# Kernel tuning notes

Measured on AMD Instinct MI355X. Metric: run time of the kernel, lower is better.

Reference implementation:

```python
import jax, jax.numpy as jnp
import numpy as np

N_NODES = 100000
N_EDGES = 1600000
D = 128
RESIDUAL_WEIGHT = 0.001


def setup_inputs() -> dict:
    key = jax.random.key(0)
    k = jax.random.split(key, 7)
    x = jax.random.normal(k[0], (N_NODES, D), dtype=jnp.float32)
    edge_index = jax.random.randint(k[1], (2, N_EDGES), 0, N_NODES, dtype=jnp.int32)
    s = 1.0 / np.sqrt(D)
    Wl = jax.random.normal(k[2], (D, D), dtype=jnp.float32) * s
    bl = jax.random.normal(k[3], (D,), dtype=jnp.float32) * s
    Wr = jax.random.normal(k[4], (D, D), dtype=jnp.float32) * s
    Wres = jax.random.normal(k[5], (D, D), dtype=jnp.float32) * s
    bres = jax.random.normal(k[6], (D,), dtype=jnp.float32) * s
    return {"x": x, "edge_index": edge_index, "Wl": Wl, "bl": bl,
            "Wr": Wr, "Wres": Wres, "bres": bres}


def reference(x, edge_index, Wl, bl, Wr, Wres, bres):
    # PyG SAGEConv(aggr='sum'): messages x_j flow src -> dst
    src, dst = edge_index[0], edge_index[1]
    agg = jax.ops.segment_sum(x[src], dst, num_segments=x.shape[0])  # [N, D]
    # lin_l(agg) (with bias) + lin_r(x) (root weight, no bias)
    h_sage = agg @ Wl.T + bl + x @ Wr.T
    # residual Linear
    h_res = x @ Wres.T + bres
    rw = jnp.float32(RESIDUAL_WEIGHT)
    # dropout p=0 (eval) -> identity
    return rw * h_sage + (1.0 - rw) * h_res
```

## Files before the change

kernel.cpp:

```cpp
#include <hip/hip_runtime.h>
#include <hip/hip_bf16.h>
#include <stdint.h>

#define DD 128
#define RW 0.001f
#define CHUNK 4096
#define CAP 4096
#define YSCALE 256.0f
#define YINV (1.0f/256.0f)

typedef __attribute__((ext_vector_type(4))) float f32x4;
typedef __attribute__((ext_vector_type(2))) float f32x2;
typedef __attribute__((ext_vector_type(8))) short bf16x8;

static __device__ __forceinline__ uint32_t pack2(float lo, float hi){
  return __builtin_amdgcn_perm(__float_as_uint(hi), __float_as_uint(lo), 0x07060302u);
}

static __device__ __forceinline__ ushort rne_bf16(float f){
  uint32_t u = __float_as_uint(f);
  return (ushort)((u + 0x7fffu + ((u >> 16) & 1u)) >> 16);
}

__global__ void prep_weights(const float* __restrict__ Wl, const float* __restrict__ bl,
                             const float* __restrict__ Wr, const float* __restrict__ Wres,
                             const float* __restrict__ bres,
                             ushort* __restrict__ Wlb, ushort* __restrict__ Wcb,
                             float* __restrict__ bc){
  int i = blockIdx.x * 256 + threadIdx.x;
  float wl = RW * Wl[i];
  float wc = RW * Wr[i] + (1.f - RW) * Wres[i];
  Wlb[i] = rne_bf16(wl);
  Wcb[i] = rne_bf16(wc);
  if (i < DD) bc[i] = RW * bl[i] + (1.f - RW) * bres[i];
}

__global__ __launch_bounds__(512) void bfill(const int* __restrict__ src,
                                             const int* __restrict__ dst,
                                             int* __restrict__ gcnt,
                                             uint32_t* __restrict__ recs, int E, int nb){
  __shared__ uint32_t srec[CHUNK];
  __shared__ uint16_t sb[CHUNK];
  __shared__ int hcnt[800];
  __shared__ int hbase[800];
  __shared__ int lcur[800];
  int t = threadIdx.x;
  int base = blockIdx.x * CHUNK;
  for (int i = t; i < nb; i += 512){ hcnt[i] = 0; lcur[i] = 0; }
  __syncthreads();
  #pragma unroll
  for (int k = 0; k < 8; k++){
    int idx = k * 512 + t;
    int e = base + idx;
    uint16_t b = 0xFFFFu;
    if (e < E){
      int d = dst[e];
      b = (uint16_t)(d >> 7);
      srec[idx] = ((uint32_t)(d & 127) << 17) | (uint32_t)src[e];
      atomicAdd(&hcnt[b], 1);
    }
    sb[idx] = b;
  }
  __syncthreads();
  for (int i = t; i < nb; i += 512)
    hbase[i] = hcnt[i] ? atomicAdd(&gcnt[i], hcnt[i]) : 0;
  __syncthreads();
  #pragma unroll
  for (int k = 0; k < 8; k++){
    int idx = k * 512 + t;
    uint16_t b = sb[idx];
    if (b != 0xFFFFu){
      int p = hbase[b] + atomicAdd(&lcur[b], 1);
      if (p < CAP) recs[(size_t)b * CAP + p] = srec[idx];
    }
  }
}

__global__ __launch_bounds__(512) void bsort(uint32_t* __restrict__ recs,
                                             const int* __restrict__ gcnt,
                                             int* __restrict__ nstart,
                                             int* __restrict__ ncnt, int M){
  __shared__ uint32_t srec[CAP];
  __shared__ uint32_t ssorted[CAP];
  __shared__ int h[128], pstart[128], lc[128];
  int t = threadIdx.x;
  int b = blockIdx.x;
  int s = b * CAP;
  int cnt = gcnt[b];
  if (cnt > CAP) cnt = CAP;

  if (t < 128){ h[t] = 0; lc[t] = 0; }
  __syncthreads();
  for (int i = t; i < cnt; i += 512){
    uint32_t r = recs[s + i];
    srec[i] = r;
    atomicAdd(&h[(r >> 17) & 127u], 1);
  }
  __syncthreads();
  int val = (t < 128) ? h[t] : 0;
  #pragma unroll
  for (int off = 1; off < 128; off <<= 1){
    if (t < 128) pstart[t] = val;
    __syncthreads();
    if (t < 128 && t >= off) val += pstart[t - off];
    __syncthreads();
  }
  if (t < 128){
    pstart[t] = val - h[t];
    int node = b * 128 + t;
    if (node < M){
      nstart[node] = s + pstart[t];
      ncnt[node]  = h[t];
    }
  }
  __syncthreads();
  for (int i = t; i < cnt; i += 512){
    uint32_t r = srec[i];
    int n7 = (int)((r >> 17) & 127u);
    int pos = pstart[n7] + atomicAdd(&lc[n7], 1);
    ssorted[pos] = r & 0x1FFFFu;
  }
  __syncthreads();
  for (int i = t; i < cnt; i += 512)
    recs[s + i] = ssorted[i];
}

__global__ __launch_bounds__(512, 4) void gemm_fused(
    const float* __restrict__ x, const ushort* __restrict__ Wlb,
    const ushort* __restrict__ Wcb, const float* __restrict__ bc,
    uint8_t* __restrict__ y, float* __restrict__ out, int M)
{
  __shared__ char sX[32768];
  int tid = threadIdx.x;

  #pragma unroll
  for (int p = 0; p < 4; p++){
    int g   = p * 512 + tid;
    int row = g >> 4;
    int cb  = (tid & 15) * 16;
    int grow = blockIdx.x * 128 + row;
    if (grow >= M) grow = M - 1;
    const float* ap = x + (size_t)grow * DD + (tid & 15) * 8;
    f32x4 f0 = *(const f32x4*)ap;
    f32x4 f1 = *(const f32x4*)(ap + 4);
    uint4 wv;
    wv.x = pack2(f0[0], f0[1]);
    wv.y = pack2(f0[2], f0[3]);
    wv.z = pack2(f1[0], f1[1]);
    wv.w = pack2(f1[2], f1[3]);
    int sw = (row << 8) | (cb ^ ((row & 7) << 4));
    *(uint4*)&sX[sw] = wv;
  }
  __syncthreads();

  int lane = tid & 63, w = tid >> 6;
  int wr = w >> 2, wc = w & 3;
  int l15 = lane & 15, lhi = lane >> 4;
  int rowbase = blockIdx.x * 128 + wr * 64;
  int mtx = wc >> 1;
  int colbase = (wc & 1) * 64;
  const ushort* Wb = mtx ? Wcb : Wlb;

  f32x4 acc[4][4];
  #pragma unroll
  for (int a = 0; a < 4; a++)
    #pragma unroll
    for (int b = 0; b < 4; b++) acc[a][b] = (f32x4){0.f,0.f,0.f,0.f};

  #pragma unroll
  for (int ks = 0; ks < 4; ks++){
    bf16x8 afr[4];
    #pragma unroll
    for (int rt = 0; rt < 4; rt++){
      int row = wr * 64 + rt * 16 + l15;
      int byte = (row << 8) | ((ks * 64 + lhi * 16) ^ ((row & 7) << 4));
      afr[rt] = *(const bf16x8*)&sX[byte];
    }
    #pragma unroll
    for (int ct = 0; ct < 4; ct++){
      int colm = colbase + ct * 16 + l15;
      bf16x8 bfr = *(const bf16x8*)(Wb + (size_t)colm * DD + ks * 32 + lhi * 8);
      #pragma unroll
      for (int rt = 0; rt < 4; rt++)
        acc[rt][ct] = __builtin_amdgcn_mfma_f32_16x16x32_bf16(bfr, afr[rt], acc[rt][ct], 0, 0, 0);
    }
  }

  if (mtx == 1){
    #pragma unroll
    for (int ct = 0; ct < 4; ct++){
      int col = colbase + ct * 16 + lhi * 4;
      f32x4 b4 = *(const f32x4*)&bc[col];
      #pragma unroll
      for (int rt = 0; rt < 4; rt++){
        int row = rowbase + rt * 16 + l15;
        if (row < M){
          f32x4 o = acc[rt][ct] + b4;
          *(f32x4*)(out + (size_t)row * DD + col) = o;
        }
      }
    }
  } else {
    #pragma unroll
    for (int ct = 0; ct < 4; ct++){
      int col = colbase + ct * 16 + lhi * 4;
      #pragma unroll
      for (int rt = 0; rt < 4; rt++){
        int row = rowbase + rt * 16 + l15;
        if (row < M){
          int pk = __builtin_amdgcn_cvt_pk_fp8_f32(acc[rt][ct][0] * YSCALE,
                                                   acc[rt][ct][1] * YSCALE, 0, false);
          pk = __builtin_amdgcn_cvt_pk_fp8_f32(acc[rt][ct][2] * YSCALE,
                                               acc[rt][ct][3] * YSCALE, pk, true);
          *(uint32_t*)(y + (size_t)row * DD + col) = (uint32_t)pk;
        }
      }
    }
  }
}

__global__ __launch_bounds__(256) void agg_add(
    const uint8_t* __restrict__ y, const uint32_t* __restrict__ csr,
    const int* __restrict__ nstart, const int* __restrict__ ncnt,
    float* __restrict__ out, int N)
{
  int wid = (int)((blockIdx.x * 256 + threadIdx.x) >> 6);
  if (wid >= N) return;
  int lane = threadIdx.x & 63;
  int start = nstart[wid], cnt = ncnt[wid];
  float a0 = 0.f, a1 = 0.f, b0 = 0.f, b1 = 0.f;
  float c0 = 0.f, c1 = 0.f, d0 = 0.f, d1 = 0.f;
  int i = 0;
  for (; i + 8 <= cnt; i += 8){
    int s0 = (int)csr[start + i];
    int s1 = (int)csr[start + i + 1];
    int s2 = (int)csr[start + i + 2];
    int s3 = (int)csr[start + i + 3];
    int s4 = (int)csr[start + i + 4];
    int s5 = (int)csr[start + i + 5];
    int s6 = (int)csr[start + i + 6];
    int s7 = (int)csr[start + i + 7];
    int v0 = *(const ushort*)(y + (size_t)s0 * DD + lane * 2);
    int v1 = *(const ushort*)(y + (size_t)s1 * DD + lane * 2);
    int v2 = *(const ushort*)(y + (size_t)s2 * DD + lane * 2);
    int v3 = *(const ushort*)(y + (size_t)s3 * DD + lane * 2);
    int v4 = *(const ushort*)(y + (size_t)s4 * DD + lane * 2);
    int v5 = *(const ushort*)(y + (size_t)s5 * DD + lane * 2);
    int v6 = *(const ushort*)(y + (size_t)s6 * DD + lane * 2);
    int v7 = *(const ushort*)(y + (size_t)s7 * DD + lane * 2);
    f32x2 f0 = __builtin_amdgcn_cvt_pk_f32_fp8(v0, false);
    f32x2 f1 = __builtin_amdgcn_cvt_pk_f32_fp8(v1, false);
    f32x2 f2 = __builtin_amdgcn_cvt_pk_f32_fp8(v2, false);
    f32x2 f3 = __builtin_amdgcn_cvt_pk_f32_fp8(v3, false);
    f32x2 f4 = __builtin_amdgcn_cvt_pk_f32_fp8(v4, false);
    f32x2 f5 = __builtin_amdgcn_cvt_pk_f32_fp8(v5, false);
    f32x2 f6 = __builtin_amdgcn_cvt_pk_f32_fp8(v6, false);
    f32x2 f7 = __builtin_amdgcn_cvt_pk_f32_fp8(v7, false);
    a0 += f0[0] + f4[0]; a1 += f0[1] + f4[1];
    b0 += f1[0] + f5[0]; b1 += f1[1] + f5[1];
    c0 += f2[0] + f6[0]; c1 += f2[1] + f6[1];
    d0 += f3[0] + f7[0]; d1 += f3[1] + f7[1];
  }
  for (; i + 2 <= cnt; i += 2){
    int s0 = (int)csr[start + i];
    int s1 = (int)csr[start + i + 1];
    int v0 = *(const ushort*)(y + (size_t)s0 * DD + lane * 2);
    int v1 = *(const ushort*)(y + (size_t)s1 * DD + lane * 2);
    f32x2 f0 = __builtin_amdgcn_cvt_pk_f32_fp8(v0, false);
    f32x2 f1 = __builtin_amdgcn_cvt_pk_f32_fp8(v1, false);
    a0 += f0[0]; a1 += f0[1];
    b0 += f1[0]; b1 += f1[1];
  }
  if (i < cnt){
    int s0 = (int)csr[start + i];
    int v0 = *(const ushort*)(y + (size_t)s0 * DD + lane * 2);
    f32x2 f0 = __builtin_amdgcn_cvt_pk_f32_fp8(v0, false);
    a0 += f0[0]; a1 += f0[1];
  }
  a0 = (a0 + b0 + c0 + d0) * YINV;
  a1 = (a1 + b1 + c1 + d1) * YINV;
  float2* p = (float2*)(out + (size_t)wid * DD + lane * 2);
  float2 t = *p;
  t.x += a0; t.y += a1;
  *p = t;
}

extern "C" void kernel_launch(void* const* d_in, const int* in_sizes, int n_in,
                              void* d_out, int out_size, void* d_ws, size_t ws_size,
                              hipStream_t stream) {
  const float* x    = (const float*)d_in[0];
  const int*   ei   = (const int*)d_in[1];
  const float* Wl   = (const float*)d_in[2];
  const float* bl   = (const float*)d_in[3];
  const float* Wr   = (const float*)d_in[4];
  const float* Wres = (const float*)d_in[5];
  const float* bres = (const float*)d_in[6];
  float* out = (float*)d_out;

  int M = in_sizes[0] / DD;
  int E = in_sizes[1] / 2;
  const int* esrc = ei;
  const int* edst = ei + E;
  int nb = (M + 127) >> 7;

  char* wsp = (char*)d_ws;
  size_t off = 0;
  uint8_t*  y    = (uint8_t*) (wsp + off); off += (size_t)M * DD;      off = (off + 255) & ~255ull;
  uint32_t* recs = (uint32_t*)(wsp + off); off += (size_t)800 * CAP * 4;
  ushort*   Wlb  = (ushort*)  (wsp + off); off += DD * DD * 2;
  ushort*   Wcb  = (ushort*)  (wsp + off); off += DD * DD * 2;
  float*    bc   = (float*)   (wsp + off); off += 512;
  int*      gcnt = (int*)     (wsp + off); off += sizeof(int) * 1024;
  int*      nstart=(int*)     (wsp + off); off += sizeof(int) * (size_t)M; off = (off + 255) & ~255ull;
  int*      ncnt = (int*)     (wsp + off); off += sizeof(int) * (size_t)M;

  hipMemsetAsync(gcnt, 0, sizeof(int) * 1024, stream);
  prep_weights<<<(DD * DD) / 256, 256, 0, stream>>>(Wl, bl, Wr, Wres, bres, Wlb, Wcb, bc);
  int nchunk = (E + CHUNK - 1) / CHUNK;
  bfill<<<nchunk, 512, 0, stream>>>(esrc, edst, gcnt, recs, E, nb);
  bsort<<<nb, 512, 0, stream>>>(recs, gcnt, nstart, ncnt, M);
  gemm_fused<<<(M + 127) / 128, 512, 0, stream>>>(x, Wlb, Wcb, bc, y, out, M);
  agg_add<<<((size_t)M * 64 + 255) / 256, 256, 0, stream>>>(y, recs, nstart, ncnt, out, M);
}
```

Before: 135.5 us.

## Aggregate quantized x before GEMM and fuse both linear maps into one kernel

Reorders the computation from transform-then-aggregate to aggregate-then-transform. x is first quantized to fp8, neighbour sums are gathered into an fp8 ybar buffer, and a single GEMM over the concatenated [x | ybar] input with a fused 128x256 weight writes the output. This drops the read-modify-write of out in the old aggregation pass, and the aggregation now splits each node's edges across two waves. In exchange it adds a quantization kernel and an extra M*128 byte intermediate, and fp8 rounding of raw x and of the summed aggregate may reduce accuracy.

```diff
diff --git a/kernel.cpp b/kernel.cpp
--- a/kernel.cpp
+++ b/kernel.cpp
@@ -6,8 +6,7 @@
 #define RW 0.001f
 #define CHUNK 4096
 #define CAP 4096
-#define YSCALE 256.0f
-#define YINV (1.0f/256.0f)
+#define YS 8.0f
 
 typedef __attribute__((ext_vector_type(4))) float f32x4;
 typedef __attribute__((ext_vector_type(2))) float f32x2;
@@ -25,14 +24,28 @@
 __global__ void prep_weights(const float* __restrict__ Wl, const float* __restrict__ bl,
                              const float* __restrict__ Wr, const float* __restrict__ Wres,
                              const float* __restrict__ bres,
-                             ushort* __restrict__ Wlb, ushort* __restrict__ Wcb,
-                             float* __restrict__ bc){
+                             ushort* __restrict__ Wfb, float* __restrict__ bc){
   int i = blockIdx.x * 256 + threadIdx.x;
-  float wl = RW * Wl[i];
-  float wc = RW * Wr[i] + (1.f - RW) * Wres[i];
-  Wlb[i] = rne_bf16(wl);
-  Wcb[i] = rne_bf16(wc);
+  int c = i >> 8, k = i & 255;
+  float v;
+  if (k < DD) v = RW * Wr[c * DD + k] + (1.f - RW) * Wres[c * DD + k];
+  else        v = (RW / YS) * Wl[c * DD + (k - DD)];
+  Wfb[i] = rne_bf16(v);
   if (i < DD) bc[i] = RW * bl[i] + (1.f - RW) * bres[i];
+}
+
+__global__ __launch_bounds__(256) void quantx(const float* __restrict__ x,
+                                              uint8_t* __restrict__ xb, int n8){
+  int i = blockIdx.x * 256 + threadIdx.x;
+  if (i >= n8) return;
+  const f32x4* p = (const f32x4*)(x + (size_t)i * 8);
+  f32x4 f0 = p[0], f1 = p[1];
+  int pk0 = __builtin_amdgcn_cvt_pk_fp8_f32(f0[0], f0[1], 0, false);
+  pk0     = __builtin_amdgcn_cvt_pk_fp8_f32(f0[2], f0[3], pk0, true);
+  int pk1 = __builtin_amdgcn_cvt_pk_fp8_f32(f1[0], f1[1], 0, false);
+  pk1     = __builtin_amdgcn_cvt_pk_fp8_f32(f1[2], f1[3], pk1, true);
+  uint2 w; w.x = (uint32_t)pk0; w.y = (uint32_t)pk1;
+  *(uint2*)(xb + (size_t)i * 8) = w;
 }
 
 __global__ __launch_bounds__(512) void bfill(const int* __restrict__ src,
@@ -125,22 +138,108 @@
     recs[s + i] = ssorted[i];
 }
 
-__global__ __launch_bounds__(512, 4) void gemm_fused(
-    const float* __restrict__ x, const ushort* __restrict__ Wlb,
-    const ushort* __restrict__ Wcb, const float* __restrict__ bc,
-    uint8_t* __restrict__ y, float* __restrict__ out, int M)
+__global__ __launch_bounds__(512) void agg(const uint8_t* __restrict__ xb,
+                                           const uint32_t* __restrict__ csr,
+                                           const int* __restrict__ nstart,
+                                           const int* __restrict__ ncnt,
+                                           uint8_t* __restrict__ ybar, int N)
+{
+  __shared__ float2 part[8][64];
+  int t = threadIdx.x;
+  int w = t >> 6, lane = t & 63;
+  int node = blockIdx.x * 4 + (w >> 1);
+  int half = w & 1;
+  float a0 = 0.f, a1 = 0.f, b0 = 0.f, b1 = 0.f;
+  float c0 = 0.f, c1 = 0.f, d0 = 0.f, d1 = 0.f;
+  if (node < N){
+    int start = nstart[node], cnt = ncnt[node];
+    int h = (cnt + 1) >> 1;
+    int i0 = start + half * h;
+    int i1 = start + cnt; if (i0 + h < i1) i1 = i0 + h;
+    int i = i0;
+    for (; i + 8 <= i1; i += 8){
+      int s0 = (int)csr[i];     int s1 = (int)csr[i + 1];
+      int s2 = (int)csr[i + 2]; int s3 = (int)csr[i + 3];
+      int s4 = (int)csr[i + 4]; int s5 = (int)csr[i + 5];
+      int s6 = (int)csr[i + 6]; int s7 = (int)csr[i + 7];
+      int v0 = *(const ushort*)(xb + (size_t)s0 * DD + lane * 2);
+      int v1 = *(const ushort*)(xb + (size_t)s1 * DD + lane * 2);
+      int v2 = *(const ushort*)(xb + (size_t)s2 * DD + lane * 2);
+      int v3 = *(const ushort*)(xb + (size_t)s3 * DD + lane * 2);
+      int v4 = *(const ushort*)(xb + (size_t)s4 * DD + lane * 2);
+      int v5 = *(const ushort*)(xb + (size_t)s5 * DD + lane * 2);
+      int v6 = *(const ushort*)(xb + (size_t)s6 * DD + lane * 2);
+      int v7 = *(const ushort*)(xb + (size_t)s7 * DD + lane * 2);
+      f32x2 f0 = __builtin_amdgcn_cvt_pk_f32_fp8(v0, false);
+      f32x2 f1 = __builtin_amdgcn_cvt_pk_f32_fp8(v1, false);
+      f32x2 f2 = __builtin_amdgcn_cvt_pk_f32_fp8(v2, false);
+      f32x2 f3 = __builtin_amdgcn_cvt_pk_f32_fp8(v3, false);
+      f32x2 f4 = __builtin_amdgcn_cvt_pk_f32_fp8(v4, false);
+      f32x2 f5 = __builtin_amdgcn_cvt_pk_f32_fp8(v5, false);
+      f32x2 f6 = __builtin_amdgcn_cvt_pk_f32_fp8(v6, false);
+      f32x2 f7 = __builtin_amdgcn_cvt_pk_f32_fp8(v7, false);
+      a0 += f0[0] + f4[0]; a1 += f0[1] + f4[1];
+      b0 += f1[0] + f5[0]; b1 += f1[1] + f5[1];
+      c0 += f2[0] + f6[0]; c1 += f2[1] + f6[1];
+      d0 += f3[0] + f7[0]; d1 += f3[1] + f7[1];
+    }
+    for (; i + 2 <= i1; i += 2){
+      int s0 = (int)csr[i];
+      int s1 = (int)csr[i + 1];
+      int v0 = *(const ushort*)(xb + (size_t)s0 * DD + lane * 2);
+      int v1 = *(const ushort*)(xb + (size_t)s1 * DD + lane * 2);
+      f32x2 f0 = __builtin_amdgcn_cvt_pk_f32_fp8(v0, false);
+      f32x2 f1 = __builtin_amdgcn_cvt_pk_f32_fp8(v1, false);
+      a0 += f0[0]; a1 += f0[1];
+      b0 += f1[0]; b1 += f1[1];
+    }
+    if (i < i1){
+      int s0 = (int)csr[i];
+      int v0 = *(const ushort*)(xb + (size_t)s0 * DD + lane * 2);
+      f32x2 f0 = __builtin_amdgcn_cvt_pk_f32_fp8(v0, false);
+      a0 += f0[0]; a1 += f0[1];
+    }
+    a0 += b0 + c0 + d0;
+    a1 += b1 + c1 + d1;
+  }
+  part[w][lane] = (float2){a0, a1};
+  __syncthreads();
+  if (half == 0 && node < N){
+    float2 o = part[w + 1][lane];
+    a0 = (a0 + o.x) * YS;
+    a1 = (a1 + o.y) * YS;
+    int pk = __builtin_amdgcn_cvt_pk_fp8_f32(a0, a1, 0, false);
+    *(ushort*)(ybar + (size_t)node * DD + lane * 2) = (ushort)(pk & 0xFFFF);
+  }
+}
+
+__global__ __launch_bounds__(512, 4) void gemm2(
+    const float* __restrict__ x, const uint8_t* __restrict__ ybar,
+    const ushort* __restrict__ Wfb, const float* __restrict__ bc,
+    float* __restrict__ out, int M)
 {
   __shared__ char sX[32768];
   int tid = threadIdx.x;
+  int lane = tid & 63, w = tid >> 6;
+  int wr = w >> 2, wcol = w & 3;
+  int l15 = lane & 15, lhi = lane >> 4;
+  int rowbase = blockIdx.x * 128 + wr * 64;
+  int colbase = wcol * 32;
+
+  f32x4 acc[4][2];
+  #pragma unroll
+  for (int a = 0; a < 4; a++)
+    #pragma unroll
+    for (int b = 0; b < 2; b++) acc[a][b] = (f32x4){0.f,0.f,0.f,0.f};
 
   #pragma unroll
   for (int p = 0; p < 4; p++){
     int g   = p * 512 + tid;
     int row = g >> 4;
-    int cb  = (tid & 15) * 16;
+    int cx  = tid & 15;
     int grow = blockIdx.x * 128 + row;
     if (grow >= M) grow = M - 1;
-    const float* ap = x + (size_t)grow * DD + (tid & 15) * 8;
+    const float* ap = x + (size_t)grow * DD + cx * 8;
     f32x4 f0 = *(const f32x4*)ap;
     f32x4 f1 = *(const f32x4*)(ap + 4);
     uint4 wv;
@@ -148,24 +247,10 @@
     wv.y = pack2(f0[2], f0[3]);
     wv.z = pack2(f1[0], f1[1]);
     wv.w = pack2(f1[2], f1[3]);
-    int sw = (row << 8) | (cb ^ ((row & 7) << 4));
+    int sw = (row << 8) | ((cx * 16) ^ ((row & 7) << 4));
     *(uint4*)&sX[sw] = wv;
   }
   __syncthreads();
-
-  int lane = tid & 63, w = tid >> 6;
-  int wr = w >> 2, wc = w & 3;
-  int l15 = lane & 15, lhi = lane >> 4;
-  int rowbase = blockIdx.x * 128 + wr * 64;
-  int mtx = wc >> 1;
-  int colbase = (wc & 1) * 64;
-  const ushort* Wb = mtx ? Wcb : Wlb;
-
-  f32x4 acc[4][4];
-  #pragma unroll
-  for (int a = 0; a < 4; a++)
-    #pragma unroll
-    for (int b = 0; b < 4; b++) acc[a][b] = (f32x4){0.f,0.f,0.f,0.f};
 
   #pragma unroll
   for (int ks = 0; ks < 4; ks++){
@@ -177,112 +262,70 @@
       afr[rt] = *(const bf16x8*)&sX[byte];
     }
     #pragma unroll
-    for (int ct = 0; ct < 4; ct++){
+    for (int ct = 0; ct < 2; ct++){
       int colm = colbase + ct * 16 + l15;
-      bf16x8 bfr = *(const bf16x8*)(Wb + (size_t)colm * DD + ks * 32 + lhi * 8);
+      bf16x8 bfr = *(const bf16x8*)(Wfb + (size_t)colm * 256 + ks * 32 + lhi * 8);
       #pragma unroll
       for (int rt = 0; rt < 4; rt++)
         acc[rt][ct] = __builtin_amdgcn_mfma_f32_16x16x32_bf16(bfr, afr[rt], acc[rt][ct], 0, 0, 0);
     }
   }
-
-  if (mtx == 1){
-    #pragma unroll
-    for (int ct = 0; ct < 4; ct++){
-      int col = colbase + ct * 16 + lhi * 4;
-      f32x4 b4 = *(const f32x4*)&bc[col];
+  __syncthreads();
+
+  #pragma unroll
+  for (int p = 0; p < 4; p++){
+    int g   = p * 512 + tid;
+    int row = g >> 4;
+    int cx  = tid & 15;
+    int grow = blockIdx.x * 128 + row;
+    if (grow >= M) grow = M - 1;
+    uint2 rv = *(const uint2*)(ybar + (size_t)grow * DD + cx * 8);
+    f32x2 e0 = __builtin_amdgcn_cvt_pk_f32_fp8((int)rv.x, false);
+    f32x2 e1 = __builtin_amdgcn_cvt_pk_f32_fp8((int)rv.x, true);
+    f32x2 e2 = __builtin_amdgcn_cvt_pk_f32_fp8((int)rv.y, false);
+    f32x2 e3 = __builtin_amdgcn_cvt_pk_f32_fp8((int)rv.y, true);
+    uint4 wv;
+    wv.x = pack2(e0[0], e0[1]);
+    wv.y = pack2(e1[0], e1[1]);
+    wv.z = pack2(e2[0], e2[1]);
+    wv.w = pack2(e3[0], e3[1]);
+    int sw = (row << 8) | ((cx * 16) ^ ((row & 7) << 4));
+    *(uint4*)&sX[sw] = wv;
+  }
+  __syncthreads();
+
+  #pragma unroll
+  for (int ks = 0; ks < 4; ks++){
+    bf16x8 afr[4];
+    #pragma unroll
+    for (int rt = 0; rt < 4; rt++){
+      int row = wr * 64 + rt * 16 + l15;
+      int byte = (row << 8) | ((ks * 64 + lhi * 16) ^ ((row & 7) << 4));
+      afr[rt] = *(const bf16x8*)&sX[byte];
+    }
+    #pragma unroll
+    for (int ct = 0; ct < 2; ct++){
+      int colm = colbase + ct * 16 + l15;
+      bf16x8 bfr = *(const bf16x8*)(Wfb + (size_t)colm * 256 + 128 + ks * 32 + lhi * 8);
       #pragma unroll
-      for (int rt = 0; rt < 4; rt++){
-        int row = rowbase + rt * 16 + l15;
-        if (row < M){
-          f32x4 o = acc[rt][ct] + b4;
-          *(f32x4*)(out + (size_t)row * DD + col) = o;
-        }
+      for (int rt = 0; rt < 4; rt++)
+        acc[rt][ct] = __builtin_amdgcn_mfma_f32_16x16x32_bf16(bfr, afr[rt], acc[rt][ct], 0, 0, 0);
+    }
+  }
+
+  #pragma unroll
+  for (int ct = 0; ct < 2; ct++){
+    int col = colbase + ct * 16 + lhi * 4;
+    f32x4 b4 = *(const f32x4*)&bc[col];
+    #pragma unroll
+    for (int rt = 0; rt < 4; rt++){
+      int row = rowbase + rt * 16 + l15;
+      if (row < M){
+        f32x4 o = acc[rt][ct] + b4;
+        *(f32x4*)(out + (size_t)row * DD + col) = o;
       }
     }
-  } else {
-    #pragma unroll
-    for (int ct = 0; ct < 4; ct++){
-      int col = colbase + ct * 16 + lhi * 4;
-      #pragma unroll
-      for (int rt = 0; rt < 4; rt++){
-        int row = rowbase + rt * 16 + l15;
-        if (row < M){
-          int pk = __builtin_amdgcn_cvt_pk_fp8_f32(acc[rt][ct][0] * YSCALE,
-                                                   acc[rt][ct][1] * YSCALE, 0, false);
-          pk = __builtin_amdgcn_cvt_pk_fp8_f32(acc[rt][ct][2] * YSCALE,
-                                               acc[rt][ct][3] * YSCALE, pk, true);
-          *(uint32_t*)(y + (size_t)row * DD + col) = (uint32_t)pk;
-        }
-      }
-    }
-  }
-}
-
-__global__ __launch_bounds__(256) void agg_add(
-    const uint8_t* __restrict__ y, const uint32_t* __restrict__ csr,
-    const int* __restrict__ nstart, const int* __restrict__ ncnt,
-    float* __restrict__ out, int N)
-{
-  int wid = (int)((blockIdx.x * 256 + threadIdx.x) >> 6);
-  if (wid >= N) return;
-  int lane = threadIdx.x & 63;
-  int start = nstart[wid], cnt = ncnt[wid];
-  float a0 = 0.f, a1 = 0.f, b0 = 0.f, b1 = 0.f;
-  float c0 = 0.f, c1 = 0.f, d0 = 0.f, d1 = 0.f;
-  int i = 0;
-  for (; i + 8 <= cnt; i += 8){
-    int s0 = (int)csr[start + i];
-    int s1 = (int)csr[start + i + 1];
-    int s2 = (int)csr[start + i + 2];
-    int s3 = (int)csr[start + i + 3];
-    int s4 = (int)csr[start + i + 4];
-    int s5 = (int)csr[start + i + 5];
-    int s6 = (int)csr[start + i + 6];
-    int s7 = (int)csr[start + i + 7];
-    int v0 = *(const ushort*)(y + (size_t)s0 * DD + lane * 2);
-    int v1 = *(const ushort*)(y + (size_t)s1 * DD + lane * 2);
-    int v2 = *(const ushort*)(y + (size_t)s2 * DD + lane * 2);
-    int v3 = *(const ushort*)(y + (size_t)s3 * DD + lane * 2);
-    int v4 = *(const ushort*)(y + (size_t)s4 * DD + lane * 2);
-    int v5 = *(const ushort*)(y + (size_t)s5 * DD + lane * 2);
-    int v6 = *(const ushort*)(y + (size_t)s6 * DD + lane * 2);
-    int v7 = *(const ushort*)(y + (size_t)s7 * DD + lane * 2);
-    f32x2 f0 = __builtin_amdgcn_cvt_pk_f32_fp8(v0, false);
-    f32x2 f1 = __builtin_amdgcn_cvt_pk_f32_fp8(v1, false);
-    f32x2 f2 = __builtin_amdgcn_cvt_pk_f32_fp8(v2, false);
-    f32x2 f3 = __builtin_amdgcn_cvt_pk_f32_fp8(v3, false);
-    f32x2 f4 = __builtin_amdgcn_cvt_pk_f32_fp8(v4, false);
-    f32x2 f5 = __builtin_amdgcn_cvt_pk_f32_fp8(v5, false);
-    f32x2 f6 = __builtin_amdgcn_cvt_pk_f32_fp8(v6, false);
-    f32x2 f7 = __builtin_amdgcn_cvt_pk_f32_fp8(v7, false);
-    a0 += f0[0] + f4[0]; a1 += f0[1] + f4[1];
-    b0 += f1[0] + f5[0]; b1 += f1[1] + f5[1];
-    c0 += f2[0] + f6[0]; c1 += f2[1] + f6[1];
-    d0 += f3[0] + f7[0]; d1 += f3[1] + f7[1];
-  }
-  for (; i + 2 <= cnt; i += 2){
-    int s0 = (int)csr[start + i];
-    int s1 = (int)csr[start + i + 1];
-    int v0 = *(const ushort*)(y + (size_t)s0 * DD + lane * 2);
-    int v1 = *(const ushort*)(y + (size_t)s1 * DD + lane * 2);
-    f32x2 f0 = __builtin_amdgcn_cvt_pk_f32_fp8(v0, false);
-    f32x2 f1 = __builtin_amdgcn_cvt_pk_f32_fp8(v1, false);
-    a0 += f0[0]; a1 += f0[1];
-    b0 += f1[0]; b1 += f1[1];
-  }
-  if (i < cnt){
-    int s0 = (int)csr[start + i];
-    int v0 = *(const ushort*)(y + (size_t)s0 * DD + lane * 2);
-    f32x2 f0 = __builtin_amdgcn_cvt_pk_f32_fp8(v0, false);
-    a0 += f0[0]; a1 += f0[1];
-  }
-  a0 = (a0 + b0 + c0 + d0) * YINV;
-  a1 = (a1 + b1 + c1 + d1) * YINV;
-  float2* p = (float2*)(out + (size_t)wid * DD + lane * 2);
-  float2 t = *p;
-  t.x += a0; t.y += a1;
-  *p = t;
+  }
 }
 
 extern "C" void kernel_launch(void* const* d_in, const int* in_sizes, int n_in,
@@ -305,20 +348,21 @@
 
   char* wsp = (char*)d_ws;
   size_t off = 0;
-  uint8_t*  y    = (uint8_t*) (wsp + off); off += (size_t)M * DD;      off = (off + 255) & ~255ull;
+  uint8_t*  xb   = (uint8_t*) (wsp + off); off += (size_t)M * DD;        off = (off + 255) & ~255ull;
+  uint8_t*  ybar = (uint8_t*) (wsp + off); off += (size_t)M * DD;        off = (off + 255) & ~255ull;
   uint32_t* recs = (uint32_t*)(wsp + off); off += (size_t)800 * CAP * 4;
-  ushort*   Wlb  = (ushort*)  (wsp + off); off += DD * DD * 2;
-  ushort*   Wcb  = (ushort*)  (wsp + off); off += DD * DD * 2;
+  ushort*   Wfb  = (ushort*)  (wsp + off); off += DD * 256 * 2;
   float*    bc   = (float*)   (wsp + off); off += 512;
   int*      gcnt = (int*)     (wsp + off); off += sizeof(int) * 1024;
   int*      nstart=(int*)     (wsp + off); off += sizeof(int) * (size_t)M; off = (off + 255) & ~255ull;
   int*      ncnt = (int*)     (wsp + off); off += sizeof(int) * (size_t)M;
 
   hipMemsetAsync(gcnt, 0, sizeof(int) * 1024, stream);
-  prep_weights<<<(DD * DD) / 256, 256, 0, stream>>>(Wl, bl, Wr, Wres, bres, Wlb, Wcb, bc);
+  prep_weights<<<(DD * 256) / 256, 256, 0, stream>>>(Wl, bl, Wr, Wres, bres, Wfb, bc);
+  quantx<<<(M * 16 + 255) / 256, 256, 0, stream>>>(x, xb, M * 16);
   int nchunk = (E + CHUNK - 1) / CHUNK;
   bfill<<<nchunk, 512, 0, stream>>>(esrc, edst, gcnt, recs, E, nb);
   bsort<<<nb, 512, 0, stream>>>(recs, gcnt, nstart, ncnt, M);
-  gemm_fused<<<(M + 127) / 128, 512, 0, stream>>>(x, Wlb, Wcb, bc, y, out, M);
-  agg_add<<<((size_t)M * 64 + 255) / 256, 256, 0, stream>>>(y, recs, nstart, ncnt, out, M);
-}
+  agg<<<(M + 3) / 4, 512, 0, stream>>>(xb, recs, nstart, ncnt, ybar, M);
+  gemm2<<<(M + 127) / 128, 512, 0, stream>>>(x, ybar, Wfb, bc, out, M);
+}
```

Measured after the change: 162.9 us. 1.2x slower.
